# Kernel optimization log

Hardware: AMD Instinct MI355X
Metric: run time of the kernel (lower is better)

Reference implementation:

```python
import jax, jax.numpy as jnp
import numpy as np

B, L, C, H = 4, 2048, 768, 12
D = C // H
MAX_SCALE_MUL = float(np.log(100.0))
BLOCK = 128  # block size for the VAR-style block-causal mask


def _block_causal_bias(L, block):
    # 0 where key-block <= query-block, -inf elsewhere (block lower-triangular)
    bid = np.arange(L) // block
    vis = bid[:, None] >= bid[None, :]
    bias = np.where(vis, 0.0, -np.inf).astype(np.float32)
    return jnp.asarray(bias)[None, None]  # (1,1,L,L)


def setup_inputs() -> dict:
    key = jax.random.key(0)
    ks = jax.random.split(key, 5)
    x = jax.random.normal(ks[0], (B, L, C), dtype=jnp.float32)
    W_qkv = jax.random.normal(ks[1], (3 * C, C), dtype=jnp.float32) * (1.0 / np.sqrt(C))
    q_bias = jnp.zeros((C,), jnp.float32)
    v_bias = jnp.zeros((C,), jnp.float32)
    # module inits scale_mul to log(4.0)
    log_scale_mul = jnp.full((1, H, 1, 1), np.log(4.0), jnp.float32)
    W_proj = jax.random.normal(ks[2], (C, C), dtype=jnp.float32) * (1.0 / np.sqrt(C))
    b_proj = jnp.zeros((C,), jnp.float32)
    attn_bias = _block_causal_bias(L, BLOCK)
    return {"x": x, "attn_bias": attn_bias, "W_qkv": W_qkv, "q_bias": q_bias,
            "v_bias": v_bias, "log_scale_mul": log_scale_mul,
            "W_proj": W_proj, "b_proj": b_proj}


def _l2norm(t, eps=1e-12):
    n = jnp.linalg.norm(t, axis=-1, keepdims=True)
    return t / jnp.maximum(n, eps)


def reference(x, attn_bias, W_qkv, q_bias, v_bias, log_scale_mul, W_proj, b_proj):
    Bx, Lx, Cx = x.shape
    # qkv projection with concatenated (q_bias, zero_k_bias, v_bias)
    bias = jnp.concatenate([q_bias, jnp.zeros_like(q_bias), v_bias])
    qkv = x @ W_qkv.T + bias                      # (B,L,3C)
    qkv = qkv.reshape(Bx, Lx, 3, H, D)
    q, k, v = jnp.moveaxis(qkv, 2, 0)             # each (B,L,H,D)
    q = jnp.swapaxes(q, 1, 2)                     # (B,H,L,D)
    k = jnp.swapaxes(k, 1, 2)
    v = jnp.swapaxes(v, 1, 2)
    # cos-attention: L2-normalize q,k; head-wise learnable scale on q; scale=1
    scale_mul = jnp.exp(jnp.minimum(log_scale_mul, MAX_SCALE_MUL))  # (1,H,1,1)
    q = _l2norm(q) * scale_mul
    k = _l2norm(k)
    scores = jnp.einsum('bhld,bhmd->bhlm', q, k) + attn_bias
    attn = jax.nn.softmax(scores, axis=-1)
    o = jnp.einsum('bhlm,bhmd->bhld', attn, v)    # (B,H,L,D)
    o = jnp.swapaxes(o, 1, 2).reshape(Bx, Lx, Cx)
    return o @ W_proj.T + b_proj
```

## Files before the change

kernel.cpp:

```cpp
#include <hip/hip_runtime.h>
#include <hip/hip_bf16.h>

#define DEV __device__ __forceinline__

typedef __bf16 bf16x8 __attribute__((ext_vector_type(8)));
typedef float  f32x4  __attribute__((ext_vector_type(4)));

typedef __attribute__((address_space(3))) unsigned int LDSU;
typedef __attribute__((address_space(1))) const unsigned int GLBU;

DEV unsigned short f2b(float f){
  __bf16 h = (__bf16)f;
  return __builtin_bit_cast(unsigned short, h);
}

static constexpr float MAXLOG = 4.60517018598809136804f;

__global__ void cvt_kernel(const float4* __restrict__ src, ushort4* __restrict__ dst, int n4){
  int i = blockIdx.x * 256 + threadIdx.x;
  if (i < n4){
    float4 v = src[i];
    ushort4 o;
    o.x = f2b(v.x); o.y = f2b(v.y); o.z = f2b(v.z); o.w = f2b(v.w);
    dst[i] = o;
  }
}

__global__ __launch_bounds__(256) void qkv_gemm(
    const unsigned short* __restrict__ X,
    const unsigned short* __restrict__ W,
    const float* __restrict__ qbias, const float* __restrict__ vbias,
    const float* __restrict__ lsm,
    unsigned short* __restrict__ Qo, unsigned short* __restrict__ Ko,
    unsigned short* __restrict__ Vo)
{
  __shared__ char smem[24576];
  char* Alds = smem;
  char* Blds = smem + 8192;

  const int tid = threadIdx.x;
  const int l = tid & 63, w = tid >> 6;
  const int wr = w >> 1, wc = w & 1;
  const int lr = l & 15, lg = l >> 4;
  const int tm = blockIdx.x % 128;
  const int tn = blockIdx.x / 128;
  const int m0 = tm * 64, n0 = tn * 128;

  f32x4 acc[2][4];
  #pragma unroll
  for (int i=0;i<2;i++)
    #pragma unroll
    for (int j=0;j<4;j++) acc[i][j] = (f32x4){0.f,0.f,0.f,0.f};

  for (int kt = 0; kt < 12; ++kt){
    const int k0 = kt * 64;
    __syncthreads();
    #pragma unroll
    for (int c = 0; c < 2; ++c){
      int chunk = c*256 + tid;
      int row = chunk >> 3;
      int scc = (chunk & 7) ^ (row & 7);
      __builtin_amdgcn_global_load_lds((GLBU*)(X + (size_t)(m0+row)*768 + k0 + scc*8),
                                       (LDSU*)(Alds + (c*256 + w*64)*16), 16, 0, 0);
    }
    #pragma unroll
    for (int c = 0; c < 4; ++c){
      int chunk = c*256 + tid;
      int row = chunk >> 3;
      int scc = (chunk & 7) ^ (row & 7);
      __builtin_amdgcn_global_load_lds((GLBU*)(W + (size_t)(n0+row)*768 + k0 + scc*8),
                                       (LDSU*)(Blds + (c*256 + w*64)*16), 16, 0, 0);
    }
    __syncthreads();
    #pragma unroll
    for (int kk = 0; kk < 2; ++kk){
      bf16x8 af[2], bfv[4];
      #pragma unroll
      for (int m=0;m<2;m++){
        int row = wr*32 + m*16 + lr;
        int byte = kk*64 + lg*16;
        af[m] = *(const bf16x8*)(Alds + row*128 + (byte ^ ((row&7)<<4)));
      }
      #pragma unroll
      for (int n=0;n<4;n++){
        int row = wc*64 + n*16 + lr;
        int byte = kk*64 + lg*16;
        bfv[n] = *(const bf16x8*)(Blds + row*128 + (byte ^ ((row&7)<<4)));
      }
      #pragma unroll
      for (int m=0;m<2;m++)
        #pragma unroll
        for (int n=0;n<4;n++)
          acc[m][n] = __builtin_amdgcn_mfma_f32_16x16x32_bf16(af[m], bfv[n], acc[m][n], 0, 0, 0);
    }
  }

  const int nb = n0 + wc*64;
  const int seg = nb / 768;
  const int h = (nb % 768) / 64;
  float smul = 1.0f;
  if (seg == 0) smul = __expf(fminf(lsm[h], MAXLOG));
  float bias_v[4];
  #pragma unroll
  for (int n=0;n<4;n++){
    int d = n*16 + lr;
    bias_v[n] = (seg==0) ? qbias[h*64+d] : (seg==2 ? vbias[h*64+d] : 0.f);
  }
  unsigned short* dst = (seg==0) ? Qo : (seg==1 ? Ko : Vo);
  #pragma unroll
  for (int m=0;m<2;m++){
    #pragma unroll
    for (int r=0;r<4;r++){
      float vals[4]; float ss = 0.f;
      #pragma unroll
      for (int n=0;n<4;n++){ float v = acc[m][n][r] + bias_v[n]; vals[n] = v; ss += v*v; }
      ss += __shfl_xor(ss,1); ss += __shfl_xor(ss,2);
      ss += __shfl_xor(ss,4); ss += __shfl_xor(ss,8);
      float sc = (seg==2) ? 1.f : smul / fmaxf(sqrtf(ss), 1e-12f);
      int grow = m0 + wr*32 + m*16 + lg*4 + r;
      int b = grow >> 11, lrow = grow & 2047;
      size_t base = (((size_t)(b*12 + h))*2048 + lrow)*64;
      #pragma unroll
      for (int n=0;n<4;n++) dst[base + n*16 + lr] = f2b(vals[n]*sc);
    }
  }
}

__global__ __launch_bounds__(512) void attn_kernel(
    const unsigned short* __restrict__ Q,
    const unsigned short* __restrict__ K,
    const unsigned short* __restrict__ V,
    const float* __restrict__ lsm,
    unsigned short* __restrict__ O)
{
  __shared__ char smem[49152];
  const int tid = threadIdx.x;
  const int l = tid & 63, w = tid >> 6;
  char* Plds = smem + 32768 + w*2048;
  const int lr = l & 15, lg = l >> 4;

  const int bid = blockIdx.x;
  const int qb = 15 - (bid / 48);
  const int bh = bid % 48;
  const int h = bh % 12;
  const size_t plane = (size_t)bh * (2048*64);
  const int q0 = qb*128 + w*16;

  const float M = __expf(fminf(lsm[h], MAXLOG));

  bf16x8 qf[2];
  #pragma unroll
  for (int ki=0;ki<2;ki++)
    qf[ki] = *(const bf16x8*)(Q + plane + (size_t)(q0 + lr)*64 + ki*32 + lg*8);

  float lsum = 0.f;
  f32x4 of[4];
  #pragma unroll
  for (int di=0;di<4;di++) of[di] = (f32x4){0.f,0.f,0.f,0.f};

  const int krow = tid >> 3;
  const int kscc = (tid & 7) ^ (krow & 7);
  const int rv  = tid & 63;
  const int c0v = (tid >> 6) * 8;

  const int nt = (qb + 1) * 2;

  {
    const unsigned short* Kt0 = K + plane;
    const unsigned short* Vt0 = V + plane;
    __builtin_amdgcn_global_load_lds((GLBU*)(Kt0 + krow*64 + kscc*8),
                                     (LDSU*)(smem + tid*16), 16, 0, 0);
    bf16x8 a = *(const bf16x8*)(Vt0 + rv*64 + c0v);
    #pragma unroll
    for (int j=0;j<8;j++)
      *(__bf16*)(smem + 16384 + (c0v+j)*128 + ((2*rv) ^ (j<<4))) = a[j];
  }

  for (int t = 0; t < nt; ++t){
    __syncthreads();
    const int pc = t & 1;
    char* Kcur = smem + pc*8192;
    char* Vcur = smem + 16384 + pc*8192;
    char* Knxt = smem + (pc^1)*8192;
    char* Vnxt = smem + 16384 + (pc^1)*8192;
    const bool pre = (t+1) < nt;

    bf16x8 nv;
    if (pre){
      const unsigned short* Kt1 = K + plane + (size_t)(t+1)*4096;
      const unsigned short* Vt1 = V + plane + (size_t)(t+1)*4096;
      __builtin_amdgcn_global_load_lds((GLBU*)(Kt1 + krow*64 + kscc*8),
                                       (LDSU*)(Knxt + tid*16), 16, 0, 0);
      nv = *(const bf16x8*)(Vt1 + rv*64 + c0v);
    }

    f32x4 s[4];
    #pragma unroll
    for (int ni=0;ni<4;ni++) s[ni] = (f32x4){0.f,0.f,0.f,0.f};
    #pragma unroll
    for (int ki=0;ki<2;ki++){
      bf16x8 kb[4];
      #pragma unroll
      for (int ni=0;ni<4;ni++){
        int key = ni*16 + lr;
        int byte = ki*64 + lg*16;
        kb[ni] = *(const bf16x8*)(Kcur + key*128 + (byte ^ ((key&7)<<4)));
      }
      #pragma unroll
      for (int ni=0;ni<4;ni++)
        s[ni] = __builtin_amdgcn_mfma_f32_16x16x32_bf16(kb[ni], qf[ki], s[ni], 0, 0, 0);
    }

    {
      const int row = lr;
      float a16 = 0.f;
      #pragma unroll
      for (int ni=0;ni<4;ni++){
        unsigned long long us = 0;
        #pragma unroll
        for (int r=0;r<4;r++){
          float p = __expf(s[ni][r] - M);
          a16 += p;
          us |= ((unsigned long long)f2b(p)) << (16*r);
        }
        *(unsigned long long*)(Plds + row*128 + ((ni*32 + lg*8) ^ ((row&7)<<4))) = us;
      }
      lsum += a16;
    }
    asm volatile("s_waitcnt lgkmcnt(0)" ::: "memory");
    __builtin_amdgcn_sched_barrier(0);

    #pragma unroll
    for (int ki=0;ki<2;ki++){
      bf16x8 pa, vbf[4];
      {
        int row = lr;
        int byte = ki*64 + lg*16;
        pa = *(const bf16x8*)(Plds + row*128 + (byte ^ ((row&7)<<4)));
      }
      #pragma unroll
      for (int di=0;di<4;di++){
        int d = di*16 + lr;
        int byte = ki*64 + lg*16;
        vbf[di] = *(const bf16x8*)(Vcur + d*128 + (byte ^ ((d&7)<<4)));
      }
      #pragma unroll
      for (int di=0;di<4;di++)
        of[di] = __builtin_amdgcn_mfma_f32_16x16x32_bf16(pa, vbf[di], of[di], 0, 0, 0);
    }

    if (pre){
      #pragma unroll
      for (int j=0;j<8;j++)
        *(__bf16*)(Vnxt + (c0v+j)*128 + ((2*rv) ^ (j<<4))) = nv[j];
    }
  }

  {
    float sum = lsum;
    sum += __shfl_xor(sum,16); sum += __shfl_xor(sum,32);
    lsum = sum;
  }
  const int b = bh / 12;
  #pragma unroll
  for (int r=0;r<4;r++){
    float inv = 1.f / __shfl(lsum, lg*4 + r);
    int row = q0 + lg*4 + r;
    size_t base = ((size_t)(b*2048) + row)*768 + h*64;
    #pragma unroll
    for (int di=0;di<4;di++)
      O[base + di*16 + lr] = f2b(of[di][r]*inv);
  }
}

__global__ __launch_bounds__(256) void proj_gemm(
    const unsigned short* __restrict__ A,
    const unsigned short* __restrict__ W,
    const float* __restrict__ bias,
    float* __restrict__ out)
{
  __shared__ char smem[16384];
  char* Alds = smem;
  char* Blds = smem + 8192;

  const int tid = threadIdx.x;
  const int l = tid & 63, w = tid >> 6;
  const int lr = l & 15, lg = l >> 4;
  const int tm = blockIdx.x % 128;
  const int tn = blockIdx.x / 128;
  const int m0 = tm * 64, n0 = tn * 64;

  f32x4 acc[4];
  #pragma unroll
  for (int j=0;j<4;j++) acc[j] = (f32x4){0.f,0.f,0.f,0.f};

  for (int kt = 0; kt < 12; ++kt){
    const int k0 = kt * 64;
    __syncthreads();
    #pragma unroll
    for (int c = 0; c < 2; ++c){
      int chunk = c*256 + tid;
      int row = chunk >> 3;
      int scc = (chunk & 7) ^ (row & 7);
      __builtin_amdgcn_global_load_lds((GLBU*)(A + (size_t)(m0+row)*768 + k0 + scc*8),
                                       (LDSU*)(Alds + (c*256 + w*64)*16), 16, 0, 0);
      __builtin_amdgcn_global_load_lds((GLBU*)(W + (size_t)(n0+row)*768 + k0 + scc*8),
                                       (LDSU*)(Blds + (c*256 + w*64)*16), 16, 0, 0);
    }
    __syncthreads();
    #pragma unroll
    for (int kk = 0; kk < 2; ++kk){
      bf16x8 af, bfv[4];
      {
        int row = w*16 + lr;
        int byte = kk*64 + lg*16;
        af = *(const bf16x8*)(Alds + row*128 + (byte ^ ((row&7)<<4)));
      }
      #pragma unroll
      for (int n=0;n<4;n++){
        int row = n*16 + lr;
        int byte = kk*64 + lg*16;
        bfv[n] = *(const bf16x8*)(Blds + row*128 + (byte ^ ((row&7)<<4)));
      }
      #pragma unroll
      for (int n=0;n<4;n++)
        acc[n] = __builtin_amdgcn_mfma_f32_16x16x32_bf16(af, bfv[n], acc[n], 0, 0, 0);
    }
  }

  #pragma unroll
  for (int r=0;r<4;r++){
    int grow = m0 + w*16 + lg*4 + r;
    #pragma unroll
    for (int n=0;n<4;n++){
      int colg = n0 + n*16 + lr;
      out[(size_t)grow*768 + colg] = acc[n][r] + bias[colg];
    }
  }
}

extern "C" void kernel_launch(void* const* d_in, const int* in_sizes, int n_in,
                              void* d_out, int out_size, void* d_ws, size_t ws_size,
                              hipStream_t stream)
{
  const float* x     = (const float*)d_in[0];
  const float* Wqkv  = (const float*)d_in[2];
  const float* qbias = (const float*)d_in[3];
  const float* vbias = (const float*)d_in[4];
  const float* lsm   = (const float*)d_in[5];
  const float* Wproj = (const float*)d_in[6];
  const float* bproj = (const float*)d_in[7];
  float* out = (float*)d_out;

  char* ws = (char*)d_ws;
  size_t off = 0;
  auto alloc = [&](size_t bytes)->char*{
    char* p = ws + off; off += (bytes + 255) & ~(size_t)255; return p;
  };
  unsigned short* xb  = (unsigned short*)alloc((size_t)8192*768*2);
  unsigned short* wqb = (unsigned short*)alloc((size_t)2304*768*2);
  unsigned short* wpb = (unsigned short*)alloc((size_t)768*768*2);
  unsigned short* qn  = (unsigned short*)alloc((size_t)48*2048*64*2);
  unsigned short* kn  = (unsigned short*)alloc((size_t)48*2048*64*2);
  unsigned short* vn  = (unsigned short*)alloc((size_t)48*2048*64*2);
  unsigned short* ob  = (unsigned short*)alloc((size_t)8192*768*2);

  cvt_kernel<<<6144, 256, 0, stream>>>((const float4*)x,     (ushort4*)xb,  1572864);
  cvt_kernel<<<1728, 256, 0, stream>>>((const float4*)Wqkv,  (ushort4*)wqb,  442368);
  cvt_kernel<<< 576, 256, 0, stream>>>((const float4*)Wproj, (ushort4*)wpb,  147456);
  qkv_gemm<<<128*18, 256, 0, stream>>>(xb, wqb, qbias, vbias, lsm, qn, kn, vn);
  attn_kernel<<<768, 512, 0, stream>>>(qn, kn, vn, lsm, ob);
  proj_gemm<<<128*12, 256, 0, stream>>>(ob, wpb, bproj, out);
}
```

Measured before the change: 129.6 us.

## Double-buffer LDS tiles and enlarge QKV GEMM tile to 128x128 with 512 threads

The QKV projection GEMM now uses 8 waves per block and a 128x128 output tile, halving the grid size. It also double-buffers the A and B tiles in 64 KB of LDS: the next K-slice is prefetched asynchronously while MFMAs run on the current one, and the second barrier per iteration is removed. The goal is to hide global-load latency and improve reuse of the weight tile. In exchange, each block needs more LDS and may run fewer blocks per CU. Correctness relies on the barrier waiting for the outstanding direct-to-LDS loads.

Result: no change. 129.1 us (-0.4%).

```diff
diff --git a/kernel.cpp b/kernel.cpp
--- a/kernel.cpp
+++ b/kernel.cpp
@@ -26,7 +26,7 @@
   }
 }
 
-__global__ __launch_bounds__(256) void qkv_gemm(
+__global__ __launch_bounds__(512) void qkv_gemm(
     const unsigned short* __restrict__ X,
     const unsigned short* __restrict__ W,
     const float* __restrict__ qbias, const float* __restrict__ vbias,
@@ -34,17 +34,14 @@
     unsigned short* __restrict__ Qo, unsigned short* __restrict__ Ko,
     unsigned short* __restrict__ Vo)
 {
-  __shared__ char smem[24576];
-  char* Alds = smem;
-  char* Blds = smem + 8192;
-
+  __shared__ char smem[65536];
   const int tid = threadIdx.x;
   const int l = tid & 63, w = tid >> 6;
   const int wr = w >> 1, wc = w & 1;
   const int lr = l & 15, lg = l >> 4;
-  const int tm = blockIdx.x % 128;
-  const int tn = blockIdx.x / 128;
-  const int m0 = tm * 64, n0 = tn * 128;
+  const int tm = blockIdx.x % 64;
+  const int tn = blockIdx.x / 64;
+  const int m0 = tm * 128, n0 = tn * 128;
 
   f32x4 acc[2][4];
   #pragma unroll
@@ -52,26 +49,39 @@
     #pragma unroll
     for (int j=0;j<4;j++) acc[i][j] = (f32x4){0.f,0.f,0.f,0.f};
 
+  #pragma unroll
+  for (int c=0;c<2;++c){
+    int chunk = c*512 + tid;
+    int row = chunk >> 3;
+    int scc = (chunk & 7) ^ (row & 7);
+    __builtin_amdgcn_global_load_lds((GLBU*)(X + (size_t)(m0+row)*768 + scc*8),
+                                     (LDSU*)(smem + chunk*16), 16, 0, 0);
+    __builtin_amdgcn_global_load_lds((GLBU*)(W + (size_t)(n0+row)*768 + scc*8),
+                                     (LDSU*)(smem + 32768 + chunk*16), 16, 0, 0);
+  }
+
   for (int kt = 0; kt < 12; ++kt){
-    const int k0 = kt * 64;
     __syncthreads();
-    #pragma unroll
-    for (int c = 0; c < 2; ++c){
-      int chunk = c*256 + tid;
-      int row = chunk >> 3;
-      int scc = (chunk & 7) ^ (row & 7);
-      __builtin_amdgcn_global_load_lds((GLBU*)(X + (size_t)(m0+row)*768 + k0 + scc*8),
-                                       (LDSU*)(Alds + (c*256 + w*64)*16), 16, 0, 0);
-    }
-    #pragma unroll
-    for (int c = 0; c < 4; ++c){
-      int chunk = c*256 + tid;
-      int row = chunk >> 3;
-      int scc = (chunk & 7) ^ (row & 7);
-      __builtin_amdgcn_global_load_lds((GLBU*)(W + (size_t)(n0+row)*768 + k0 + scc*8),
-                                       (LDSU*)(Blds + (c*256 + w*64)*16), 16, 0, 0);
-    }
-    __syncthreads();
+    const int pc = kt & 1;
+    char* Acur = smem + pc*16384;
+    char* Bcur = smem + 32768 + pc*16384;
+
+    if (kt + 1 < 12){
+      const int k1 = (kt+1)*64;
+      char* Anxt = smem + (pc^1)*16384;
+      char* Bnxt = smem + 32768 + (pc^1)*16384;
+      #pragma unroll
+      for (int c=0;c<2;++c){
+        int chunk = c*512 + tid;
+        int row = chunk >> 3;
+        int scc = (chunk & 7) ^ (row & 7);
+        __builtin_amdgcn_global_load_lds((GLBU*)(X + (size_t)(m0+row)*768 + k1 + scc*8),
+                                         (LDSU*)(Anxt + chunk*16), 16, 0, 0);
+        __builtin_amdgcn_global_load_lds((GLBU*)(W + (size_t)(n0+row)*768 + k1 + scc*8),
+                                         (LDSU*)(Bnxt + chunk*16), 16, 0, 0);
+      }
+    }
+
     #pragma unroll
     for (int kk = 0; kk < 2; ++kk){
       bf16x8 af[2], bfv[4];
@@ -79,13 +89,13 @@
       for (int m=0;m<2;m++){
         int row = wr*32 + m*16 + lr;
         int byte = kk*64 + lg*16;
-        af[m] = *(const bf16x8*)(Alds + row*128 + (byte ^ ((row&7)<<4)));
+        af[m] = *(const bf16x8*)(Acur + row*128 + (byte ^ ((row&7)<<4)));
       }
       #pragma unroll
       for (int n=0;n<4;n++){
         int row = wc*64 + n*16 + lr;
         int byte = kk*64 + lg*16;
-        bfv[n] = *(const bf16x8*)(Blds + row*128 + (byte ^ ((row&7)<<4)));
+        bfv[n] = *(const bf16x8*)(Bcur + row*128 + (byte ^ ((row&7)<<4)));
       }
       #pragma unroll
       for (int m=0;m<2;m++)
@@ -368,7 +378,7 @@
   cvt_kernel<<<6144, 256, 0, stream>>>((const float4*)x,     (ushort4*)xb,  1572864);
   cvt_kernel<<<1728, 256, 0, stream>>>((const float4*)Wqkv,  (ushort4*)wqb,  442368);
   cvt_kernel<<< 576, 256, 0, stream>>>((const float4*)Wproj, (ushort4*)wpb,  147456);
-  qkv_gemm<<<128*18, 256, 0, stream>>>(xb, wqb, qbias, vbias, lsm, qn, kn, vn);
+  qkv_gemm<<<64*18, 512, 0, stream>>>(xb, wqb, qbias, vbias, lsm, qn, kn, vn);
   attn_kernel<<<768, 512, 0, stream>>>(qn, kn, vn, lsm, ob);
   proj_gemm<<<128*12, 256, 0, stream>>>(ob, wpb, bproj, out);
 }
```
